# Kernel optimization log

Measured on AMD Instinct MI355X. Metric: run time of the kernel, lower is better.

The kernel has to match this reference:

```python
import jax, jax.numpy as jnp
import numpy as np

B, T, S, E, H = 2, 2048, 2048, 1024, 16
HD = E // H  # 64


def setup_inputs() -> dict:
    key = jax.random.key(0)
    ks = jax.random.split(key, 13)
    sc = 1.0 / np.sqrt(E)
    inp = {
        "q": jax.random.normal(ks[0], (B, T, E), jnp.float32),
        "k": jax.random.normal(ks[1], (B, S, E), jnp.float32),
        "v": jax.random.normal(ks[2], (B, S, E), jnp.float32),
        "attn_mask": jax.random.randint(ks[3], (T, S), 0, 2, jnp.int32),
        "Wq": jax.random.normal(ks[4], (E, E), jnp.float32) * sc,
        "bq": jax.random.normal(ks[5], (E,), jnp.float32) * 0.01,
        "Wk": jax.random.normal(ks[6], (E, E), jnp.float32) * sc,
        "bk": jax.random.normal(ks[7], (E,), jnp.float32) * 0.01,
        "Wv": jax.random.normal(ks[8], (E, E), jnp.float32) * sc,
        "bv": jax.random.normal(ks[9], (E,), jnp.float32) * 0.01,
        "Wo": jax.random.normal(ks[10], (E, E), jnp.float32) * sc,
        "bo": jax.random.normal(ks[11], (E,), jnp.float32) * 0.01,
    }
    return inp


def reference(q, k, v, attn_mask, Wq, bq, Wk, bk, Wv, bv, Wo, bo):
    bsz, tgt_len, embed_dim = q.shape
    src_len = k.shape[1]
    # torch Linear: x @ W.T + b
    qh = (q @ Wq.T + bq).reshape(bsz, tgt_len, H, HD).transpose(0, 2, 1, 3)  # [B,H,T,HD]
    kh = (k @ Wk.T + bk).reshape(bsz, src_len, H, HD).transpose(0, 2, 1, 3)  # [B,H,S,HD]
    vh = (v @ Wv.T + bv).reshape(bsz, src_len, H, HD).transpose(0, 2, 1, 3)  # [B,H,S,HD]
    scale = 1.0 / jnp.sqrt(jnp.asarray(HD, qh.dtype))
    attn = jnp.einsum('bhtd,bhsd->bhts', qh, kh) * scale  # [B,H,T,S]
    attn = jnp.where(attn_mask != 0, jnp.asarray(-10000.0, attn.dtype), attn)
    attn = jax.nn.softmax(attn, axis=-1)
    out = jnp.einsum('bhts,bhsd->bhtd', attn, vh)  # [B,H,T,HD]
    out = out.transpose(0, 2, 1, 3).reshape(bsz, tgt_len, embed_dim)
    return out @ Wo.T + bo
```

## Files before the change

### kernel.cpp

```cpp
#include <hip/hip_runtime.h>
#include <hip/hip_bf16.h>
#include <math.h>

#define QSCALE 0.18033688011112042f

typedef __attribute__((ext_vector_type(4))) float f32x4;
typedef __attribute__((ext_vector_type(8))) short bf16x8;
typedef __attribute__((ext_vector_type(4))) short bf16x4;
typedef __attribute__((ext_vector_type(4))) float float4_t;
typedef __attribute__((ext_vector_type(4))) int int4_t;
typedef __attribute__((ext_vector_type(2))) unsigned int uint2_t;
typedef __attribute__((ext_vector_type(2))) unsigned long long u64x2;

typedef const __attribute__((address_space(1))) void gbl_cvoid;
typedef __attribute__((address_space(3))) void lds_void;

static __device__ __forceinline__ void gload16(const void* g, void* l){
  __builtin_amdgcn_global_load_lds((gbl_cvoid*)g, (lds_void*)l, 16, 0, 0);
}

static __device__ __forceinline__ unsigned short f2b(float f){
  unsigned int u = __builtin_bit_cast(unsigned int, f);
  u = (u + 0x7FFFu + ((u >> 16) & 1u)) >> 16;
  return (unsigned short)u;
}

static __device__ __forceinline__ unsigned int cvtpk_bf16(float a, float b){
  unsigned int r;
  asm("v_cvt_pk_bf16_f32 %0, %1, %2" : "=v"(r) : "v"(a), "v"(b));
  return r;
}

#if defined(__has_builtin)
#if __has_builtin(__builtin_amdgcn_exp2f)
#define EXP2R __builtin_amdgcn_exp2f
#endif
#endif
#ifndef EXP2R
#define EXP2R exp2f
#endif

struct CvtArgs { const float* src[7]; unsigned short* dst[7]; };

__global__ __launch_bounds__(256) void cvt_kernel(CvtArgs a, const int* __restrict__ mask,
                                                  unsigned long long* __restrict__ mout){
  int y = blockIdx.y;
  if (y == 7){
    if (blockIdx.x >= 256) return;
    int w = blockIdx.x * 256 + threadIdx.x;
    const int* p = mask + (size_t)w * 64;
    unsigned long long bits = 0ull;
    #pragma unroll
    for (int j = 0; j < 64; j += 4){
      int4_t v4 = *(const int4_t*)(p + j);
      if (v4[0]) bits |= (1ull << (j + 0));
      if (v4[1]) bits |= (1ull << (j + 1));
      if (v4[2]) bits |= (1ull << (j + 2));
      if (v4[3]) bits |= (1ull << (j + 3));
    }
    mout[w] = bits;
    return;
  }
  int n4 = (y < 3) ? (4194304/4) : (1048576/4);
  int idx = blockIdx.x * 256 + threadIdx.x;
  if (idx >= n4) return;
  float4_t v = *(const float4_t*)(a.src[y] + (size_t)idx * 4);
  bf16x4 b; b[0]=(short)f2b(v[0]); b[1]=(short)f2b(v[1]); b[2]=(short)f2b(v[2]); b[3]=(short)f2b(v[3]);
  *(bf16x4*)(a.dst[y] + (size_t)idx * 4) = b;
}

struct GemmArgs { const unsigned short* A[3]; const unsigned short* W[3];
                  const float* bias[3]; void* C[3]; };

__global__ __launch_bounds__(256) void gemm_qkv_kernel(GemmArgs ga)
{
  __shared__ unsigned short As[128*64];
  __shared__ unsigned short Ws[128*64];
  const int tid = threadIdx.x, lane = tid & 63, wid = tid >> 6;
  const int sel = blockIdx.y >> 3;
  const int n0  = (blockIdx.y & 7) * 128;
  const int m0  = blockIdx.x * 128;
  const unsigned short* A = ga.A[sel];
  const unsigned short* W = ga.W[sel];
  const float* bias = ga.bias[sel];
  const int wm = wid >> 1, wn = wid & 1;
  const int r16 = lane & 15, kg = lane >> 4;
  const int x7 = r16 & 7;
  const int sR = tid >> 3;
  const int sL = (tid & 7) ^ (sR & 7);

  f32x4 acc[4][4];
  const f32x4 z4 = {0.f, 0.f, 0.f, 0.f};
  #pragma unroll
  for (int i = 0; i < 4; ++i)
    #pragma unroll
    for (int j = 0; j < 4; ++j) acc[i][j] = z4;

  for (int k0 = 0; k0 < 1024; k0 += 64) {
    #pragma unroll
    for (int i = 0; i < 4; ++i){
      int row = i * 32 + sR;
      gload16(A + (size_t)(m0 + row) * 1024 + k0 + sL * 8, (char*)As + i * 4096 + wid * 1024);
      gload16(W + (size_t)(n0 + row) * 1024 + k0 + sL * 8, (char*)Ws + i * 4096 + wid * 1024);
    }
    __syncthreads();
    #pragma unroll
    for (int kk = 0; kk < 2; ++kk){
      bf16x8 af[4], wf[4];
      #pragma unroll
      for (int mi = 0; mi < 4; ++mi)
        af[mi] = *(const bf16x8*)(As + (wm*64 + mi*16 + r16)*64 + (((kk<<2) + kg) ^ x7)*8);
      #pragma unroll
      for (int ni = 0; ni < 4; ++ni)
        wf[ni] = *(const bf16x8*)(Ws + (wn*64 + ni*16 + r16)*64 + (((kk<<2) + kg) ^ x7)*8);
      #pragma unroll
      for (int mi = 0; mi < 4; ++mi)
        #pragma unroll
        for (int ni = 0; ni < 4; ++ni)
          acc[mi][ni] = __builtin_amdgcn_mfma_f32_16x16x32_bf16(af[mi], wf[ni], acc[mi][ni], 0, 0, 0);
    }
    __syncthreads();
  }

  #pragma unroll
  for (int mi = 0; mi < 4; ++mi){
    #pragma unroll
    for (int ni = 0; ni < 4; ++ni){
      int m = m0 + wm*64 + mi*16 + kg*4;
      int n = n0 + wn*64 + ni*16 + r16;
      float bv = bias[n];
      if (sel == 2){
        int bb = m >> 11, t = m & 2047, hh = n >> 6, d = n & 63;
        bf16x4 pk;
        #pragma unroll
        for (int r = 0; r < 4; ++r) pk[r] = (short)f2b(acc[mi][ni][r] + bv);
        *(bf16x4*)&((unsigned short*)ga.C[2])[((size_t)(bb*16 + hh) * 64 + d) * 2048 + t] = pk;
      } else {
        #pragma unroll
        for (int r = 0; r < 4; ++r){
          float v = acc[mi][ni][r] + bv;
          if (sel == 0) v *= QSCALE;
          int mm = m + r;
          int bb = mm >> 11, t = mm & 2047, hh = n >> 6, d = n & 63;
          ((unsigned short*)ga.C[sel])[(((size_t)(bb*16 + hh) * 2048 + t) << 6) + d] = f2b(v);
        }
      }
    }
  }
}

__global__ __launch_bounds__(256) void gemm_o_kernel(const unsigned short* __restrict__ A,
    const unsigned short* __restrict__ W, const float* __restrict__ bias,
    float* __restrict__ C)
{
  __shared__ unsigned short As[64*64];
  __shared__ unsigned short Ws[128*64];
  const int tid = threadIdx.x, lane = tid & 63, wid = tid >> 6;
  const int m0 = blockIdx.x * 64;
  const int n0 = blockIdx.y * 128;
  const int wm = wid >> 1, wn = wid & 1;
  const int r16 = lane & 15, kg = lane >> 4;
  const int x7 = r16 & 7;
  const int sR = tid >> 3;
  const int sL = (tid & 7) ^ (sR & 7);

  f32x4 acc[2][4];
  const f32x4 z4 = {0.f, 0.f, 0.f, 0.f};
  #pragma unroll
  for (int i = 0; i < 2; ++i)
    #pragma unroll
    for (int j = 0; j < 4; ++j) acc[i][j] = z4;

  for (int k0 = 0; k0 < 1024; k0 += 64) {
    #pragma unroll
    for (int i = 0; i < 2; ++i){
      int row = i * 32 + sR;
      gload16(A + (size_t)(m0 + row) * 1024 + k0 + sL * 8, (char*)As + i * 4096 + wid * 1024);
    }
    #pragma unroll
    for (int i = 0; i < 4; ++i){
      int row = i * 32 + sR;
      gload16(W + (size_t)(n0 + row) * 1024 + k0 + sL * 8, (char*)Ws + i * 4096 + wid * 1024);
    }
    __syncthreads();
    #pragma unroll
    for (int kk = 0; kk < 2; ++kk){
      bf16x8 af[2], wf[4];
      #pragma unroll
      for (int mi = 0; mi < 2; ++mi)
        af[mi] = *(const bf16x8*)(As + (wm*32 + mi*16 + r16)*64 + (((kk<<2) + kg) ^ x7)*8);
      #pragma unroll
      for (int ni = 0; ni < 4; ++ni)
        wf[ni] = *(const bf16x8*)(Ws + (wn*64 + ni*16 + r16)*64 + (((kk<<2) + kg) ^ x7)*8);
      #pragma unroll
      for (int mi = 0; mi < 2; ++mi)
        #pragma unroll
        for (int ni = 0; ni < 4; ++ni)
          acc[mi][ni] = __builtin_amdgcn_mfma_f32_16x16x32_bf16(af[mi], wf[ni], acc[mi][ni], 0, 0, 0);
    }
    __syncthreads();
  }

  #pragma unroll
  for (int mi = 0; mi < 2; ++mi){
    #pragma unroll
    for (int ni = 0; ni < 4; ++ni){
      int m = m0 + wm*32 + mi*16 + kg*4;
      int n = n0 + wn*64 + ni*16 + r16;
      float bv = bias[n];
      #pragma unroll
      for (int r = 0; r < 4; ++r)
        C[(size_t)(m + r) * 1024 + n] = acc[mi][ni][r] + bv;
    }
  }
}

__global__ __launch_bounds__(512) void attn_kernel(const unsigned short* __restrict__ qh,
    const unsigned short* __restrict__ kh, const unsigned short* __restrict__ vhT,
    const unsigned long long* __restrict__ mbits, unsigned short* __restrict__ attnout)
{
  __shared__ short Ks[2][2][64][64];
  __shared__ short Vs[2][2][64][64];
  __shared__ short Ps[128][64];
  const int tid = threadIdx.x, lane = tid & 63, wid = tid >> 6;
  const int bh = blockIdx.y;
  const int b = bh >> 4, h = bh & 15;
  const int t0 = blockIdx.x * 128;
  const int tw = t0 + wid * 16;
  const int r16 = lane & 15, kg = lane >> 4;
  const int x7 = r16 & 7;
  const int ph0 = (kg ^ x7) * 8;
  const int ph1 = ((kg + 4) ^ x7) * 8;
  const int sR = tid >> 3;
  const int sL = (tid & 7) ^ (sR & 7);

  const unsigned short* kbase = kh + (size_t)bh * 2048 * 64;
  const unsigned short* vtb   = vhT + (size_t)bh * 64 * 2048;
  const unsigned short* qbase = qh + ((size_t)bh * 2048 + tw) * 64;

  bf16x8 aq[2];
  aq[0] = *(const bf16x8*)(qbase + (size_t)r16 * 64 + kg * 8);
  aq[1] = *(const bf16x8*)(qbase + (size_t)r16 * 64 + 32 + kg * 8);

  const short ob = (short)0x3F80;
  const bf16x8 ones8 = {ob, ob, ob, ob, ob, ob, ob, ob};

  f32x4 o[4], o5;
  const f32x4 z4 = {0.f, 0.f, 0.f, 0.f};
  #pragma unroll
  for (int df = 0; df < 4; ++df) o[df] = z4;
  o5 = z4;

  const unsigned long long* mrow = mbits + (size_t)(tw + r16) * 32;
  const size_t koff = (size_t)sR * 64 + sL * 8;
  const size_t voff = (size_t)sR * 2048 + sL * 8;

  #pragma unroll
  for (int i = 0; i < 2; ++i){
    gload16(kbase + (size_t)i * 4096 + koff, (char*)Ks + i * 8192 + wid * 1024);
    gload16(vtb + voff + i * 64,            (char*)Vs + i * 8192 + wid * 1024);
  }
  u64x2 mw = *(const u64x2*)(mrow);
  __syncthreads();

#define ATTN_STEP(CUR, IT)                                                            \
  {                                                                                   \
    u64x2 mwn = mw;                                                                   \
    if ((IT) < 15) {                                                                  \
      const unsigned short* kc = kbase + (size_t)((IT) + 1) * 8192;                   \
      const unsigned short* vc = vtb + (size_t)((IT) + 1) * 128;                      \
      _Pragma("unroll")                                                               \
      for (int i = 0; i < 2; ++i){                                                    \
        gload16(kc + (size_t)i * 4096 + koff,                                         \
                (char*)Ks + ((CUR) ^ 1) * 16384 + i * 8192 + wid * 1024);             \
        gload16(vc + voff + i * 64,                                                   \
                (char*)Vs + ((CUR) ^ 1) * 16384 + i * 8192 + wid * 1024);             \
      }                                                                               \
      mwn = *(const u64x2*)(mrow + 2 * ((IT) + 1));                                   \
    }                                                                                 \
    _Pragma("unroll")                                                                 \
    for (int sub = 0; sub < 2; ++sub){                                                \
      f32x4 sfr[4];                                                                   \
      __builtin_amdgcn_s_setprio(1);                                                  \
      _Pragma("unroll")                                                               \
      for (int sb = 0; sb < 4; ++sb){                                                 \
        bf16x8 bk0 = *(const bf16x8*)&Ks[CUR][sub][sb*16 + r16][ph0];                 \
        bf16x8 bk1 = *(const bf16x8*)&Ks[CUR][sub][sb*16 + r16][ph1];                 \
        f32x4 z = z4;                                                                 \
        z = __builtin_amdgcn_mfma_f32_16x16x32_bf16(bk0, aq[0], z, 0, 0, 0);          \
        z = __builtin_amdgcn_mfma_f32_16x16x32_bf16(bk1, aq[1], z, 0, 0, 0);          \
        sfr[sb] = z;                                                                  \
      }                                                                               \
      __builtin_amdgcn_s_setprio(0);                                                  \
      {                                                                               \
        unsigned long long mk = (~mw[sub]) >> (kg * 4);                 \
        unsigned int wlo = (unsigned int)mk;                                          \
        unsigned int whi = (unsigned int)(mk >> 32);                                  \
        _Pragma("unroll")                                                             \
        for (int sb = 0; sb < 4; ++sb){                                               \
          unsigned int wd = (sb < 2) ? wlo : whi;                                     \
          float pf[4];                                                                \
          _Pragma("unroll")                                                           \
          for (int r = 0; r < 4; ++r){                                                \
            const int pos = (sb & 1) * 16 + r;                                        \
            unsigned int msk = (unsigned int)((int)(wd << (31 - pos)) >> 31);         \
            float e = EXP2R(sfr[sb][r]);                                              \
            pf[r] = __builtin_bit_cast(float,                                         \
                      __builtin_bit_cast(unsigned int, e) & msk);                     \
          }                                                                           \
          unsigned int lo = cvtpk_bf16(pf[0], pf[1]);                                 \
          unsigned int hi = cvtpk_bf16(pf[2], pf[3]);                                 \
          int phys = (sb * 2 + (kg >> 1)) ^ x7;                                       \
          uint2_t pk; pk[0] = lo; pk[1] = hi;                                         \
          *(uint2_t*)&Ps[wid*16 + r16][phys * 8 + (kg & 1) * 4] = pk;                 \
        }                                                                             \
      }                                                                               \
      bf16x8 pa0 = *(const bf16x8*)&Ps[wid*16 + r16][ph0];                            \
      bf16x8 pa1 = *(const bf16x8*)&Ps[wid*16 + r16][ph1];                            \
      __builtin_amdgcn_s_setprio(1);                                                  \
      _Pragma("unroll")                                                               \
      for (int df = 0; df < 4; ++df){                                                 \
        bf16x8 bv0 = *(const bf16x8*)&Vs[CUR][sub][df*16 + r16][ph0];                 \
        bf16x8 bv1 = *(const bf16x8*)&Vs[CUR][sub][df*16 + r16][ph1];                 \
        o[df] = __builtin_amdgcn_mfma_f32_16x16x32_bf16(pa0, bv0, o[df], 0, 0, 0);    \
        o[df] = __builtin_amdgcn_mfma_f32_16x16x32_bf16(pa1, bv1, o[df], 0, 0, 0);    \
      }                                                                               \
      o5 = __builtin_amdgcn_mfma_f32_16x16x32_bf16(pa0, ones8, o5, 0, 0, 0);          \
      o5 = __builtin_amdgcn_mfma_f32_16x16x32_bf16(pa1, ones8, o5, 0, 0, 0);          \
      __builtin_amdgcn_s_setprio(0);                                                  \
    }                                                                                 \
    __syncthreads();                                                                  \
    mw = mwn;                                                                         \
  }

  for (int ii = 0; ii < 8; ++ii) {
    ATTN_STEP(0, 2 * ii)
    ATTN_STEP(1, 2 * ii + 1)
  }
#undef ATTN_STEP

  float lv0 = 1.0f / o5[0];
  float lv1 = 1.0f / o5[1];
  float lv2 = 1.0f / o5[2];
  float lv3 = 1.0f / o5[3];
  #pragma unroll
  for (int df = 0; df < 4; ++df){
    int col = h*64 + df*16 + r16;
    int t = tw + kg*4;
    attnout[(size_t)(b * 2048 + t + 0) * 1024 + col] = (short)f2b(o[df][0] * lv0);
    attnout[(size_t)(b * 2048 + t + 1) * 1024 + col] = (short)f2b(o[df][1] * lv1);
    attnout[(size_t)(b * 2048 + t + 2) * 1024 + col] = (short)f2b(o[df][2] * lv2);
    attnout[(size_t)(b * 2048 + t + 3) * 1024 + col] = (short)f2b(o[df][3] * lv3);
  }
}

extern "C" void kernel_launch(void* const* d_in, const int* in_sizes, int n_in,
                              void* d_out, int out_size, void* d_ws, size_t ws_size,
                              hipStream_t stream) {
  const float* q    = (const float*)d_in[0];
  const float* k    = (const float*)d_in[1];
  const float* v    = (const float*)d_in[2];
  const int*   mask = (const int*)d_in[3];
  const float* Wq = (const float*)d_in[4];  const float* bq = (const float*)d_in[5];
  const float* Wk = (const float*)d_in[6];  const float* bk = (const float*)d_in[7];
  const float* Wv = (const float*)d_in[8];  const float* bv = (const float*)d_in[9];
  const float* Wo = (const float*)d_in[10]; const float* bo = (const float*)d_in[11];

  char* ws = (char*)d_ws;
  unsigned short* qb   = (unsigned short*)(ws);
  unsigned short* kb   = (unsigned short*)(ws + 8388608);
  unsigned short* vb   = (unsigned short*)(ws + 16777216);
  unsigned short* Wqb  = (unsigned short*)(ws + 25165824);
  unsigned short* Wkb  = (unsigned short*)(ws + 27262976);
  unsigned short* Wvb  = (unsigned short*)(ws + 29360128);
  unsigned short* Wob  = (unsigned short*)(ws + 31457280);
  unsigned short* qhd  = (unsigned short*)(ws + 33554432);
  unsigned short* khd  = (unsigned short*)(ws + 41943040);
  unsigned short* vhT  = (unsigned short*)(ws + 50331648);
  unsigned long long* mbits = (unsigned long long*)(ws + 58720256);
  unsigned short* attno = qb;

  CvtArgs ca;
  ca.src[0]=q;  ca.dst[0]=qb;  ca.src[1]=k;  ca.dst[1]=kb;  ca.src[2]=v;  ca.dst[2]=vb;
  ca.src[3]=Wq; ca.dst[3]=Wqb; ca.src[4]=Wk; ca.dst[4]=Wkb;
  ca.src[5]=Wv; ca.dst[5]=Wvb; ca.src[6]=Wo; ca.dst[6]=Wob;
  cvt_kernel<<<dim3(4096, 8), 256, 0, stream>>>(ca, mask, mbits);

  GemmArgs g0;
  g0.A[0]=qb; g0.A[1]=kb; g0.A[2]=vb;
  g0.W[0]=Wqb; g0.W[1]=Wkb; g0.W[2]=Wvb;
  g0.bias[0]=bq; g0.bias[1]=bk; g0.bias[2]=bv;
  g0.C[0]=qhd; g0.C[1]=khd; g0.C[2]=vhT;
  gemm_qkv_kernel<<<dim3(32, 24), 256, 0, stream>>>(g0);

  attn_kernel<<<dim3(16, 32), 512, 0, stream>>>(qhd, khd, vhT, mbits, attno);

  gemm_o_kernel<<<dim3(64, 8), 256, 0, stream>>>(attno, Wob, bo, (float*)d_out);
}
```

Baseline: 136.6 us.

## Double-buffer LDS in QKV and output projection GEMMs with BK=32 prefetch

Both projection GEMMs now use two 32-wide K tiles in shared memory. The next tile's global-to-LDS load is issued before the current tile's MFMAs, and the swizzle is adjusted for the 32-element row stride. The goal is to hide global load latency behind compute and drop one barrier per step. In exchange the K step is halved, so there are twice as many iterations and barriers, with less MFMA work between each sync.

```diff
diff --git a/kernel.cpp b/kernel.cpp
--- a/kernel.cpp
+++ b/kernel.cpp
@@ -74,8 +74,8 @@
 
 __global__ __launch_bounds__(256) void gemm_qkv_kernel(GemmArgs ga)
 {
-  __shared__ unsigned short As[128*64];
-  __shared__ unsigned short Ws[128*64];
+  __shared__ unsigned short As[2*128*32];
+  __shared__ unsigned short Ws[2*128*32];
   const int tid = threadIdx.x, lane = tid & 63, wid = tid >> 6;
   const int sel = blockIdx.y >> 3;
   const int n0  = (blockIdx.y & 7) * 128;
@@ -85,9 +85,9 @@
   const float* bias = ga.bias[sel];
   const int wm = wid >> 1, wn = wid & 1;
   const int r16 = lane & 15, kg = lane >> 4;
-  const int x7 = r16 & 7;
-  const int sR = tid >> 3;
-  const int sL = (tid & 7) ^ (sR & 7);
+  const int phA = (kg ^ ((r16 >> 1) & 3)) * 8;
+  const int sRow = tid >> 2;
+  const int sL   = (tid & 3) ^ ((tid >> 3) & 3);
 
   f32x4 acc[4][4];
   const f32x4 z4 = {0.f, 0.f, 0.f, 0.f};
@@ -96,31 +96,46 @@
     #pragma unroll
     for (int j = 0; j < 4; ++j) acc[i][j] = z4;
 
-  for (int k0 = 0; k0 < 1024; k0 += 64) {
-    #pragma unroll
-    for (int i = 0; i < 4; ++i){
-      int row = i * 32 + sR;
-      gload16(A + (size_t)(m0 + row) * 1024 + k0 + sL * 8, (char*)As + i * 4096 + wid * 1024);
-      gload16(W + (size_t)(n0 + row) * 1024 + k0 + sL * 8, (char*)Ws + i * 4096 + wid * 1024);
-    }
-    __syncthreads();
-    #pragma unroll
-    for (int kk = 0; kk < 2; ++kk){
-      bf16x8 af[4], wf[4];
-      #pragma unroll
-      for (int mi = 0; mi < 4; ++mi)
-        af[mi] = *(const bf16x8*)(As + (wm*64 + mi*16 + r16)*64 + (((kk<<2) + kg) ^ x7)*8);
-      #pragma unroll
-      for (int ni = 0; ni < 4; ++ni)
-        wf[ni] = *(const bf16x8*)(Ws + (wn*64 + ni*16 + r16)*64 + (((kk<<2) + kg) ^ x7)*8);
-      #pragma unroll
-      for (int mi = 0; mi < 4; ++mi)
-        #pragma unroll
-        for (int ni = 0; ni < 4; ++ni)
-          acc[mi][ni] = __builtin_amdgcn_mfma_f32_16x16x32_bf16(af[mi], wf[ni], acc[mi][ni], 0, 0, 0);
-    }
-    __syncthreads();
-  }
+  #pragma unroll
+  for (int i = 0; i < 2; ++i){
+    gload16(A + (size_t)(m0 + i*64 + sRow) * 1024 + sL * 8, (char*)As + i*4096 + wid*1024);
+    gload16(W + (size_t)(n0 + i*64 + sRow) * 1024 + sL * 8, (char*)Ws + i*4096 + wid*1024);
+  }
+  __syncthreads();
+
+#define GSTEP(CUR, IT)                                                                \
+  {                                                                                   \
+    if ((IT) < 31) {                                                                  \
+      const int k1 = ((IT) + 1) * 32;                                                 \
+      _Pragma("unroll")                                                               \
+      for (int i = 0; i < 2; ++i){                                                    \
+        gload16(A + (size_t)(m0 + i*64 + sRow) * 1024 + k1 + sL * 8,                  \
+                (char*)As + ((CUR) ^ 1) * 8192 + i*4096 + wid*1024);                  \
+        gload16(W + (size_t)(n0 + i*64 + sRow) * 1024 + k1 + sL * 8,                  \
+                (char*)Ws + ((CUR) ^ 1) * 8192 + i*4096 + wid*1024);                  \
+      }                                                                               \
+    }                                                                                 \
+    bf16x8 af[4], wf[4];                                                              \
+    _Pragma("unroll")                                                                 \
+    for (int mi = 0; mi < 4; ++mi)                                                    \
+      af[mi] = *(const bf16x8*)(As + (CUR)*4096 + (wm*64 + mi*16 + r16)*32 + phA);    \
+    _Pragma("unroll")                                                                 \
+    for (int ni = 0; ni < 4; ++ni)                                                    \
+      wf[ni] = *(const bf16x8*)(Ws + (CUR)*4096 + (wn*64 + ni*16 + r16)*32 + phA);    \
+    _Pragma("unroll")                                                                 \
+    for (int mi = 0; mi < 4; ++mi)                                                    \
+      _Pragma("unroll")                                                               \
+      for (int ni = 0; ni < 4; ++ni)                                                  \
+        acc[mi][ni] = __builtin_amdgcn_mfma_f32_16x16x32_bf16(af[mi], wf[ni],         \
+                                                              acc[mi][ni], 0, 0, 0); \
+    __syncthreads();                                                                  \
+  }
+
+  for (int ii = 0; ii < 16; ++ii) {
+    GSTEP(0, 2 * ii)
+    GSTEP(1, 2 * ii + 1)
+  }
+#undef GSTEP
 
   #pragma unroll
   for (int mi = 0; mi < 4; ++mi){
@@ -153,16 +168,16 @@
     const unsigned short* __restrict__ W, const float* __restrict__ bias,
     float* __restrict__ C)
 {
-  __shared__ unsigned short As[64*64];
-  __shared__ unsigned short Ws[128*64];
+  __shared__ unsigned short As[2*64*32];
+  __shared__ unsigned short Ws[2*128*32];
   const int tid = threadIdx.x, lane = tid & 63, wid = tid >> 6;
   const int m0 = blockIdx.x * 64;
   const int n0 = blockIdx.y * 128;
   const int wm = wid >> 1, wn = wid & 1;
   const int r16 = lane & 15, kg = lane >> 4;
-  const int x7 = r16 & 7;
-  const int sR = tid >> 3;
-  const int sL = (tid & 7) ^ (sR & 7);
+  const int phA = (kg ^ ((r16 >> 1) & 3)) * 8;
+  const int sRow = tid >> 2;
+  const int sL   = (tid & 3) ^ ((tid >> 3) & 3);
 
   f32x4 acc[2][4];
   const f32x4 z4 = {0.f, 0.f, 0.f, 0.f};
@@ -171,35 +186,44 @@
     #pragma unroll
     for (int j = 0; j < 4; ++j) acc[i][j] = z4;
 
-  for (int k0 = 0; k0 < 1024; k0 += 64) {
-    #pragma unroll
-    for (int i = 0; i < 2; ++i){
-      int row = i * 32 + sR;
-      gload16(A + (size_t)(m0 + row) * 1024 + k0 + sL * 8, (char*)As + i * 4096 + wid * 1024);
-    }
-    #pragma unroll
-    for (int i = 0; i < 4; ++i){
-      int row = i * 32 + sR;
-      gload16(W + (size_t)(n0 + row) * 1024 + k0 + sL * 8, (char*)Ws + i * 4096 + wid * 1024);
-    }
-    __syncthreads();
-    #pragma unroll
-    for (int kk = 0; kk < 2; ++kk){
-      bf16x8 af[2], wf[4];
-      #pragma unroll
-      for (int mi = 0; mi < 2; ++mi)
-        af[mi] = *(const bf16x8*)(As + (wm*32 + mi*16 + r16)*64 + (((kk<<2) + kg) ^ x7)*8);
-      #pragma unroll
-      for (int ni = 0; ni < 4; ++ni)
-        wf[ni] = *(const bf16x8*)(Ws + (wn*64 + ni*16 + r16)*64 + (((kk<<2) + kg) ^ x7)*8);
-      #pragma unroll
-      for (int mi = 0; mi < 2; ++mi)
-        #pragma unroll
-        for (int ni = 0; ni < 4; ++ni)
-          acc[mi][ni] = __builtin_amdgcn_mfma_f32_16x16x32_bf16(af[mi], wf[ni], acc[mi][ni], 0, 0, 0);
-    }
-    __syncthreads();
-  }
+  gload16(A + (size_t)(m0 + sRow) * 1024 + sL * 8, (char*)As + wid*1024);
+  #pragma unroll
+  for (int i = 0; i < 2; ++i)
+    gload16(W + (size_t)(n0 + i*64 + sRow) * 1024 + sL * 8, (char*)Ws + i*4096 + wid*1024);
+  __syncthreads();
+
+#define OSTEP(CUR, IT)                                                                \
+  {                                                                                   \
+    if ((IT) < 31) {                                                                  \
+      const int k1 = ((IT) + 1) * 32;                                                 \
+      gload16(A + (size_t)(m0 + sRow) * 1024 + k1 + sL * 8,                           \
+              (char*)As + ((CUR) ^ 1) * 4096 + wid*1024);                             \
+      _Pragma("unroll")                                                               \
+      for (int i = 0; i < 2; ++i)                                                     \
+        gload16(W + (size_t)(n0 + i*64 + sRow) * 1024 + k1 + sL * 8,                  \
+                (char*)Ws + ((CUR) ^ 1) * 8192 + i*4096 + wid*1024);                  \
+    }                                                                                 \
+    bf16x8 af[2], wf[4];                                                              \
+    _Pragma("unroll")                                                                 \
+    for (int mi = 0; mi < 2; ++mi)                                                    \
+      af[mi] = *(const bf16x8*)(As + (CUR)*2048 + (wm*32 + mi*16 + r16)*32 + phA);    \
+    _Pragma("unroll")                                                                 \
+    for (int ni = 0; ni < 4; ++ni)                                                    \
+      wf[ni] = *(const bf16x8*)(Ws + (CUR)*4096 + (wn*64 + ni*16 + r16)*32 + phA);    \
+    _Pragma("unroll")                                                                 \
+    for (int mi = 0; mi < 2; ++mi)                                                    \
+      _Pragma("unroll")                                                               \
+      for (int ni = 0; ni < 4; ++ni)                                                  \
+        acc[mi][ni] = __builtin_amdgcn_mfma_f32_16x16x32_bf16(af[mi], wf[ni],         \
+                                                              acc[mi][ni], 0, 0, 0); \
+    __syncthreads();                                                                  \
+  }
+
+  for (int ii = 0; ii < 16; ++ii) {
+    OSTEP(0, 2 * ii)
+    OSTEP(1, 2 * ii + 1)
+  }
+#undef OSTEP
 
   #pragma unroll
   for (int mi = 0; mi < 2; ++mi){
```

New measurement: 152.1 us. 11.4% more time.
